# Kernel optimization log

Hardware: AMD Instinct MI355X
Metric: run time of the kernel (lower is better)

## Reference

```python
import jax, jax.numpy as jnp
import numpy as np

N = 30000      # nodes
E = 480000     # edges
NF = 92        # node features
EF = 50        # edge features
D1 = 64        # dim1
D2 = 64        # dim2
L = 3          # conv_count
FC = 2         # fc_count
G = 256        # graphs in batch
EPS = 1e-5


def setup_inputs() -> dict:
    key = jax.random.key(0)
    ks = jax.random.split(key, 20)
    s = 0.05
    zd = 2 * D1 + EF  # CGConv concat dim
    inp = {
        "x": jax.random.normal(ks[0], (N, NF), jnp.float32),
        "edge_attr": jax.random.uniform(ks[1], (E, EF), jnp.float32),
        "lin0_w": jax.random.normal(ks[2], (NF, D1), jnp.float32) * s,
        "lin0_b": jnp.zeros((D1,), jnp.float32),
        "conv_wf": jax.random.normal(ks[3], (L, zd, D1), jnp.float32) * s,
        "conv_bf": jnp.zeros((L, D1), jnp.float32),
        "conv_ws": jax.random.normal(ks[4], (L, zd, D1), jnp.float32) * s,
        "conv_bs": jnp.zeros((L, D1), jnp.float32),
        "bn_gamma": jnp.ones((L, D1), jnp.float32),
        "bn_beta": jnp.zeros((L, D1), jnp.float32),
        "lin1_w": jax.random.normal(ks[5], (D1, D2), jnp.float32) * s,
        "lin1_b": jnp.zeros((D2,), jnp.float32),
        "fc_w": jax.random.normal(ks[6], (FC, D2, D2), jnp.float32) * s,
        "fc_b": jnp.zeros((FC, D2), jnp.float32),
        "lin2_w": jax.random.normal(ks[7], (D2, 1), jnp.float32) * s,
        "lin2_b": jnp.zeros((1,), jnp.float32),
        "edge_index": jax.random.randint(ks[8], (2, E), 0, N),
        "batch": jnp.sort(jax.random.randint(ks[9], (N,), 0, G)),
        "n_graphs": G,
    }
    return inp


def reference(x, edge_attr, lin0_w, lin0_b, conv_wf, conv_bf, conv_ws, conv_bs,
              bn_gamma, bn_beta, lin1_w, lin1_b, fc_w, fc_b, lin2_w, lin2_b,
              edge_index, batch, n_graphs):
    n = x.shape[0]
    src = edge_index[0]  # x_j (source)
    dst = edge_index[1]  # x_i (target, aggregation index)
    h = jax.nn.relu(x @ lin0_w + lin0_b)  # [N, D1]

    # per-target edge counts for mean aggregation (constant across layers)
    cnt = jax.ops.segment_sum(jnp.ones((src.shape[0],), h.dtype), dst, num_segments=n)
    cnt = jnp.maximum(cnt, 1.0)[:, None]

    for l in range(L):
        # z = [x_i || x_j || e_ij]  -> gated message sigmoid(Wf z) * softplus(Ws z)
        z = jnp.concatenate([h[dst], h[src], edge_attr], axis=-1)  # [E, 2*D1+EF]
        m = jax.nn.sigmoid(z @ conv_wf[l] + conv_bf[l]) * jax.nn.softplus(z @ conv_ws[l] + conv_bs[l])
        aggr = jax.ops.segment_sum(m, dst, num_segments=n) / cnt  # mean aggr [N, D1]
        # BatchNorm (training-mode batch stats, biased variance as in torch)
        mu = jnp.mean(aggr, axis=0)
        var = jnp.var(aggr, axis=0)
        aggr = (aggr - mu) * jax.lax.rsqrt(var + EPS) * bn_gamma[l] + bn_beta[l]
        h = jax.nn.relu(h + aggr)  # residual then outer ReLU

    # global mean pool over graphs
    gcnt = jnp.maximum(jax.ops.segment_sum(jnp.ones((n,), h.dtype), batch, num_segments=n_graphs), 1.0)[:, None]
    out = jax.ops.segment_sum(h, batch, num_segments=n_graphs) / gcnt  # [G, D1]

    out = jax.nn.relu(out @ lin1_w + lin1_b)
    for f in range(FC):
        out = jax.nn.relu(out @ fc_w[f] + fc_b[f])
    out = out @ lin2_w + lin2_b
    return out.reshape(-1)  # [G]
```

## Files before the change

kernel.cpp:

```cpp
#include <hip/hip_runtime.h>
#include <hip/hip_bf16.h>

#define N_NODES 30000
#define N_EDGES 480000
#define NFEAT 92
#define EFEAT 50
#define D1 64
#define ZD 178
#define NL 3
#define NG 256
#define BN_EPS 1e-5f
#define NTILES (N_EDGES / 16)
#define EDGE_BLOCKS 7500
#define EDGE_GRID 7504

#define LIN0_BLOCKS 512
#define CNT_BLOCKS 1875
#define WPREP_BLOCKS 96
#define SCAN_BLOCKS ((N_NODES + 255) / 256)
#define BUILD_BLOCKS 1875
#define NP_BLOCKS 1024

typedef __attribute__((ext_vector_type(8))) short bf16x8;
typedef __attribute__((ext_vector_type(8))) unsigned short u16x8;
typedef __attribute__((ext_vector_type(4))) unsigned short u16x4;
typedef __attribute__((ext_vector_type(4))) float f32x4;

static __device__ __forceinline__ unsigned short f2bf(float v) {
  __hip_bfloat16 b = __float2bfloat16(v);
  return *(unsigned short*)&b;
}
static __device__ __forceinline__ float bfu(unsigned short u) {
  union { unsigned int i; float f; } c;
  c.i = ((unsigned int)u) << 16;
  return c.f;
}

static __device__ __forceinline__ void nodeproj_body(
    int blk0, int nblk, const float* __restrict__ hin, float* __restrict__ hout,
    const float* __restrict__ wfp, const float* __restrict__ wsm,
    unsigned short* __restrict__ projd_pk, unsigned short* __restrict__ projs_pk,
    const float* __restrict__ aggr, float* __restrict__ aggr_z,
    const float* __restrict__ invc, const float* __restrict__ musum,
    const float* __restrict__ sqsum, const float* __restrict__ gamma,
    const float* __restrict__ beta, int do_bn, float (*hl)[64]) {
  const int lane = threadIdx.x & 63;
  const int w = threadIdx.x >> 6;
  const float* W = (w < 2) ? wfp : wsm;
  const int roff = (w & 1) * 64;
  float wreg[D1];
#pragma unroll
  for (int k = 0; k < D1; ++k) wreg[k] = W[(size_t)(roff + k) * D1 + lane];
  unsigned short* pk = (w & 1) ? projs_pk : projd_pk;
  const int slot = (w < 2) ? 0 : 4;
  const int poff = (lane >> 2) * 8 + (lane & 3) + slot;
  float r = 0.0f, sh = 0.0f;
  if (do_bn) {
    const float mu = musum[lane] * (1.0f / N_NODES);
    const float var = sqsum[lane] * (1.0f / N_NODES) - mu * mu;
    r = gamma[lane] * rsqrtf(var + BN_EPS);
    sh = beta[lane] - mu * r;
  }
  for (int i = blk0; i < N_NODES; i += nblk) {
    float hv = hin[(size_t)i * D1 + lane];
    if (do_bn) {
      const float av = aggr[(size_t)i * D1 + lane] * invc[i];
      hv = fmaxf(hv + fmaf(av, r, sh), 0.0f);
      if (w == 0) hout[(size_t)i * D1 + lane] = hv;
    }
    if (w == 1) aggr_z[(size_t)i * D1 + lane] = 0.0f;
    hl[w][lane] = hv;
    __builtin_amdgcn_wave_barrier();
    const float4* hr = (const float4*)&hl[w][0];
    float acc = 0.0f;
#pragma unroll
    for (int k4 = 0; k4 < D1 / 4; ++k4) {
      const float4 v = hr[k4];
      acc = fmaf(v.x, wreg[4 * k4 + 0], acc);
      acc = fmaf(v.y, wreg[4 * k4 + 1], acc);
      acc = fmaf(v.z, wreg[4 * k4 + 2], acc);
      acc = fmaf(v.w, wreg[4 * k4 + 3], acc);
    }
    pk[(size_t)i * 128 + poff] = f2bf(acc);
    __builtin_amdgcn_wave_barrier();
  }
}

extern "C" __global__ void __launch_bounds__(256)
k_init(const float* __restrict__ x, const float* __restrict__ w,
       const float* __restrict__ b, float* __restrict__ h,
       const int* __restrict__ ei, int* __restrict__ cnt,
       const float* __restrict__ conv_wf, const float* __restrict__ conv_ws,
       unsigned short* __restrict__ Bp) {
  const int blk = blockIdx.x;
  if (blk < LIN0_BLOCKS) {
    const int lane = threadIdx.x & 63;
    const int wave = (blk * 256 + threadIdx.x) >> 6;
    const int nw = (LIN0_BLOCKS * 256) >> 6;
    float wreg[NFEAT];
#pragma unroll
    for (int k = 0; k < NFEAT; ++k) wreg[k] = w[k * D1 + lane];
    const float bj = b[lane];
    for (int i = wave; i < N_NODES; i += nw) {
      const float2* xr = (const float2*)(x + (size_t)i * NFEAT);
      float acc = bj;
#pragma unroll
      for (int k = 0; k < NFEAT / 2; ++k) {
        const float2 v = xr[k];
        acc = fmaf(v.x, wreg[2 * k], acc);
        acc = fmaf(v.y, wreg[2 * k + 1], acc);
      }
      h[(size_t)i * D1 + lane] = fmaxf(acc, 0.0f);
    }
  } else if (blk < LIN0_BLOCKS + CNT_BLOCKS) {
    const int e = (blk - LIN0_BLOCKS) * 256 + threadIdx.x;
    if (e < N_EDGES) atomicAdd(&cnt[ei[N_EDGES + e]], 1);
  } else {
    const int idx = (blk - LIN0_BLOCKS - CNT_BLOCKS) * 256 + threadIdx.x;
    const int j = idx & 7;
    const int lane = (idx >> 3) & 63;
    const int frag = (idx >> 9) & 15;
    const int l = idx >> 13;
    const int n = frag & 3;
    const int t = (frag >> 2) & 1;
    const int m = frag >> 3;
    const int k = t * 32 + (lane >> 4) * 8 + j;
    const int feat = (lane & 15) * 4 + n;
    float v = 0.0f;
    if (k < EFEAT) {
      const float* W = (m == 0) ? conv_wf : conv_ws;
      v = W[(size_t)l * ZD * D1 + (size_t)(128 + k) * D1 + feat];
    }
    Bp[idx] = f2bf(v);
  }
}

extern "C" __global__ void __launch_bounds__(256)
k_scan1(const int* __restrict__ cnt, int* __restrict__ lpre, int* __restrict__ ptot) {
  const int t = threadIdx.x;
  const int idx = blockIdx.x * 256 + t;
  const int v = (idx < N_NODES) ? cnt[idx] : 0;
  __shared__ int bs[256];
  bs[t] = v;
  __syncthreads();
  for (int off = 1; off < 256; off <<= 1) {
    int u = (t >= off) ? bs[t - off] : 0;
    __syncthreads();
    bs[t] += u;
    __syncthreads();
  }
  if (idx < N_NODES) lpre[idx] = bs[t] - v;
  if (t == 255) ptot[blockIdx.x] = bs[255];
}

extern "C" __global__ void __launch_bounds__(256)
k_scan23(const int* __restrict__ cnt, const int* __restrict__ lpre,
         const int* __restrict__ ptot, const int* __restrict__ batch,
         int* __restrict__ wptr, float* __restrict__ invc,
         int* __restrict__ grp) {
  __shared__ int bs[128];
  const int t = threadIdx.x;
  if (t < 128) bs[t] = (t < SCAN_BLOCKS) ? ptot[t] : 0;
  __syncthreads();
  for (int off = 1; off < 128; off <<= 1) {
    int u = 0;
    if (t < 128 && t >= off) u = bs[t - off];
    __syncthreads();
    if (t < 128 && t >= off) bs[t] += u;
    __syncthreads();
  }
  const int idx = blockIdx.x * 256 + t;
  if (idx >= N_NODES) return;
  const int bid = idx >> 8;
  const int boff = (bid == 0) ? 0 : bs[bid - 1];
  wptr[idx] = boff + lpre[idx];
  invc[idx] = 1.0f / fmaxf((float)cnt[idx], 1.0f);
  const int bt = batch[idx];
  if (idx == 0)
    for (int g = 0; g <= bt; ++g) grp[g] = 0;
  else {
    const int pb = batch[idx - 1];
    for (int g = pb + 1; g <= bt; ++g) grp[g] = idx;
  }
  if (idx == N_NODES - 1)
    for (int g = bt + 1; g <= NG; ++g) grp[g] = N_NODES;
}

extern "C" __global__ void __launch_bounds__(256)
k_build(const int* __restrict__ ei, int* __restrict__ wptr,
        int2* __restrict__ ds2, const float* __restrict__ ea,
        unsigned short* __restrict__ eapb,
        const float* __restrict__ h0, const float* __restrict__ wfl,
        const float* __restrict__ wsl, unsigned short* __restrict__ projd_pk,
        unsigned short* __restrict__ projs_pk, float* __restrict__ aggrA) {
  __shared__ __align__(16) int lpos[256];
  if (blockIdx.x >= BUILD_BLOCKS) {
    nodeproj_body(blockIdx.x - BUILD_BLOCKS, NP_BLOCKS, h0, nullptr, wfl, wsl,
                  projd_pk, projs_pk, nullptr, aggrA, nullptr, nullptr, nullptr,
                  nullptr, nullptr, 0, (float(*)[64])lpos);
    return;
  }
  const int e0 = blockIdx.x * 256;
  {
    const int e = e0 + threadIdx.x;
    const int d = ei[N_EDGES + e];
    const int pos = atomicAdd(&wptr[d], 1);
    ds2[pos] = make_int2(d, ei[e]);
    lpos[threadIdx.x] = pos;
  }
  __syncthreads();
  const int l16 = threadIdx.x & 15;
  const int sub = threadIdx.x >> 4;
#pragma unroll
  for (int r = 0; r < 16; ++r) {
    const int eb = r * 16 + sub;
    const size_t ge = e0 + eb;
    const int pos = lpos[eb];
    unsigned short o0 = 0, o1 = 0, o2 = 0, o3 = 0;
    if (l16 < 12) {
      const float4 v = *(const float4*)(ea + ge * EFEAT + l16 * 4);
      o0 = f2bf(v.x); o1 = f2bf(v.y); o2 = f2bf(v.z); o3 = f2bf(v.w);
    } else if (l16 == 12) {
      const float2 v = *(const float2*)(ea + ge * EFEAT + 48);
      o0 = f2bf(v.x); o1 = f2bf(v.y);
    }
    u16x4 st;
    st[0] = o0; st[1] = o1; st[2] = o2; st[3] = o3;
    *(u16x4*)(eapb + ((size_t)pos << 6) + l16 * 4) = st;
  }
}

extern "C" __global__ void __launch_bounds__(256)
k_nodeproj(const float* __restrict__ hin, float* __restrict__ hout,
           const float* __restrict__ wfp, const float* __restrict__ wsm,
           unsigned short* __restrict__ projd_pk, unsigned short* __restrict__ projs_pk,
           const float* __restrict__ aggr, float* __restrict__ aggr_z,
           const float* __restrict__ invc,
           const float* __restrict__ musum, const float* __restrict__ sqsum,
           const float* __restrict__ gamma, const float* __restrict__ beta) {
  __shared__ float hl[4][64];
  nodeproj_body(blockIdx.x, gridDim.x, hin, hout, wfp, wsm, projd_pk, projs_pk,
                aggr, aggr_z, invc, musum, sqsum, gamma, beta, 1, hl);
}

extern "C" __global__ void __launch_bounds__(256)
k_edgemm(const unsigned short* __restrict__ projd_pk,
         const unsigned short* __restrict__ projs_pk,
         const unsigned short* __restrict__ eapb,
         const int2* __restrict__ ds2,
         const unsigned short* __restrict__ Bp,
         const float* __restrict__ bfp, const float* __restrict__ bsp,
         float* __restrict__ aggr, float* __restrict__ musum,
         float* __restrict__ sqsum) {
  const int lane = threadIdx.x & 63;
  const int wv = threadIdx.x >> 6;
  const int col = lane & 15;
  const int quad = lane >> 4;
  __shared__ float mlds[4][16][68];

  const int vbid = (blockIdx.x & 7) * 938 + (blockIdx.x >> 3);
  if (blockIdx.x == 0 && wv == 0) {
    musum[lane] = 0.0f;
    sqsum[lane] = 0.0f;
  }
  if (vbid >= EDGE_BLOCKS) return;

  const int t = vbid * 4 + wv;
  const int base = t * 16;

  const int4 p01 = *(const int4*)(ds2 + base + quad * 4);
  const int4 p23 = *(const int4*)(ds2 + base + quad * 4 + 2);
  const int dr[4] = {p01.x, p01.z, p23.x, p23.z};
  const int sr[4] = {p01.y, p01.w, p23.y, p23.w};
  const bf16x8 Af0 = *(const bf16x8*)(eapb + ((size_t)(base + col) << 6) + quad * 8);
  const bf16x8 Af1 = *(const bf16x8*)(eapb + ((size_t)(base + col) << 6) + 32 + quad * 8);

  bf16x8 Bf[2][2][4];
#pragma unroll
  for (int m = 0; m < 2; ++m)
#pragma unroll
    for (int tt = 0; tt < 2; ++tt)
#pragma unroll
      for (int n = 0; n < 4; ++n)
        Bf[m][tt][n] = *(const bf16x8*)(Bp + ((((m * 2 + tt) * 4 + n) * 64 + lane) * 8));

  const f32x4 bf4 = *(const f32x4*)(bfp + col * 4);
  const f32x4 bs4 = *(const f32x4*)(bsp + col * 4);

  f32x4 aF[4], aS[4];
#pragma unroll
  for (int r = 0; r < 4; ++r) {
    const int d = dr[r];
    const int s = sr[r];
    const u16x8 pd = *(const u16x8*)(projd_pk + (size_t)d * 128 + col * 8);
    const u16x8 ss = *(const u16x8*)(projs_pk + (size_t)s * 128 + col * 8);
#pragma unroll
    for (int n = 0; n < 4; ++n) {
      aF[n][r] = bfu(pd[n]) + bfu(ss[n]) + bf4[n];
      aS[n][r] = bfu(pd[n + 4]) + bfu(ss[n + 4]) + bs4[n];
    }
  }

#pragma unroll
  for (int n = 0; n < 4; ++n) {
    aF[n] = __builtin_amdgcn_mfma_f32_16x16x32_bf16(Af0, Bf[0][0][n], aF[n], 0, 0, 0);
    aF[n] = __builtin_amdgcn_mfma_f32_16x16x32_bf16(Af1, Bf[0][1][n], aF[n], 0, 0, 0);
    aS[n] = __builtin_amdgcn_mfma_f32_16x16x32_bf16(Af0, Bf[1][0][n], aS[n], 0, 0, 0);
    aS[n] = __builtin_amdgcn_mfma_f32_16x16x32_bf16(Af1, Bf[1][1][n], aS[n], 0, 0, 0);
  }

#pragma unroll
  for (int r = 0; r < 4; ++r) {
    f32x4 mv;
#pragma unroll
    for (int n = 0; n < 4; ++n) {
      const float af = aF[n][r];
      const float as = aS[n][r];
      const float sg = __builtin_amdgcn_rcpf(1.0f + __expf(-af));
      const float sp = fmaxf(as, 0.0f) + __logf(1.0f + __expf(-fabsf(as)));
      mv[n] = sg * sp;
    }
    *(f32x4*)&mlds[wv][quad * 4 + r][col * 4] = mv;
  }
  __builtin_amdgcn_wave_barrier();

  float sum = 0.0f;
  int dcur = ds2[base].x;
#pragma unroll
  for (int p = 0; p < 16; ++p) {
    sum += mlds[wv][p][lane];
    const int dnxt = (p < 15) ? ds2[base + p + 1].x : -1;
    if (dnxt != dcur) {
      atomicAdd(&aggr[(size_t)dcur * D1 + lane], sum);
      sum = 0.0f;
      dcur = dnxt;
    }
  }
}

extern "C" __global__ void __launch_bounds__(256)
k_stats(const float* __restrict__ aggr, const float* __restrict__ invc,
        float* __restrict__ musum, float* __restrict__ sqsum) {
  const int j = threadIdx.x & 63;
  const int rid = (blockIdx.x * blockDim.x + threadIdx.x) >> 6;
  const int rstr = (gridDim.x * blockDim.x) >> 6;
  float s = 0.0f, sq = 0.0f;
  for (int i = rid; i < N_NODES; i += rstr) {
    const float v = aggr[(size_t)i * D1 + j] * invc[i];
    s += v;
    sq = fmaf(v, v, sq);
  }
  __shared__ float ls[256], lq[256];
  ls[threadIdx.x] = s;
  lq[threadIdx.x] = sq;
  __syncthreads();
  if (threadIdx.x < 64) {
    s = ls[j] + ls[64 + j] + ls[128 + j] + ls[192 + j];
    sq = lq[j] + lq[64 + j] + lq[128 + j] + lq[192 + j];
    atomicAdd(&musum[j], s);
    atomicAdd(&sqsum[j], sq);
  }
}

extern "C" __global__ void __launch_bounds__(256)
k_poolmlp(const float* __restrict__ h, const float* __restrict__ aggr,
          const float* __restrict__ invc,
          const float* __restrict__ musum, const float* __restrict__ sqsum,
          const float* __restrict__ gamma, const float* __restrict__ beta,
          const int* __restrict__ grp,
          const float* __restrict__ lin1_w, const float* __restrict__ lin1_b,
          const float* __restrict__ fc_w, const float* __restrict__ fc_b,
          const float* __restrict__ lin2_w, const float* __restrict__ lin2_b,
          float* __restrict__ out) {
  const int g = blockIdx.x;
  const int lane = threadIdx.x & 63;
  const int wv = threadIdx.x >> 6;
  const float mu = musum[lane] * (1.0f / N_NODES);
  const float var = sqsum[lane] * (1.0f / N_NODES) - mu * mu;
  const float r = gamma[lane] * rsqrtf(var + BN_EPS);
  const float sh = beta[lane] - mu * r;
  const int s = grp[g], e = grp[g + 1];
  float acc = 0.0f;
  for (int i = s + wv; i < e; i += 4) {
    const float hv = h[(size_t)i * D1 + lane];
    const float av = aggr[(size_t)i * D1 + lane] * invc[i];
    acc += fmaxf(hv + fmaf(av, r, sh), 0.0f);
  }
  __shared__ float red[4][64];
  __shared__ float vin[64];
  red[wv][lane] = acc;
  __syncthreads();
  const int j = threadIdx.x;
  float v = 0.0f;
  if (j < 64) {
    const float inv = 1.0f / fmaxf((float)(e - s), 1.0f);
    v = (red[0][j] + red[1][j] + red[2][j] + red[3][j]) * inv;
  }
  for (int layer = 0; layer < 3; ++layer) {
    if (j < 64) vin[j] = v;
    __syncthreads();
    if (j < 64) {
      const float* W;
      const float* B;
      if (layer == 0) {
        W = lin1_w;
        B = lin1_b;
      } else {
        W = fc_w + (size_t)(layer - 1) * D1 * D1;
        B = fc_b + (size_t)(layer - 1) * D1;
      }
      float a2 = B[j];
#pragma unroll 16
      for (int k = 0; k < D1; ++k) a2 = fmaf(vin[k], W[k * D1 + j], a2);
      v = fmaxf(a2, 0.0f);
    }
    __syncthreads();
  }
  if (j < 64) {
    float p = v * lin2_w[j];
#pragma unroll
    for (int off = 32; off > 0; off >>= 1) p += __shfl_down(p, off);
    if (j == 0) out[g] = p + lin2_b[0];
  }
}

extern "C" void kernel_launch(void* const* d_in, const int* in_sizes, int n_in,
                              void* d_out, int out_size, void* d_ws, size_t ws_size,
                              hipStream_t stream) {
  const float* x        = (const float*)d_in[0];
  const float* ea       = (const float*)d_in[1];
  const float* lin0_w   = (const float*)d_in[2];
  const float* lin0_b   = (const float*)d_in[3];
  const float* conv_wf  = (const float*)d_in[4];
  const float* conv_bf  = (const float*)d_in[5];
  const float* conv_ws  = (const float*)d_in[6];
  const float* conv_bs  = (const float*)d_in[7];
  const float* bn_gamma = (const float*)d_in[8];
  const float* bn_beta  = (const float*)d_in[9];
  const float* lin1_w   = (const float*)d_in[10];
  const float* lin1_b   = (const float*)d_in[11];
  const float* fc_w     = (const float*)d_in[12];
  const float* fc_b     = (const float*)d_in[13];
  const float* lin2_w   = (const float*)d_in[14];
  const float* lin2_b   = (const float*)d_in[15];
  const int*   ei       = (const int*)d_in[16];
  const int*   batch    = (const int*)d_in[17];

  uintptr_t p = (uintptr_t)d_ws;
  auto alloc = [&](size_t bytes) {
    p = (p + 255) & ~(size_t)255;
    void* r = (void*)p;
    p += bytes;
    return r;
  };
  float* h0     = (float*)alloc((size_t)N_NODES * 64 * 4);
  float* h1     = (float*)alloc((size_t)N_NODES * 64 * 4);
  unsigned short* projd_pk = (unsigned short*)alloc((size_t)N_NODES * 128 * 2);
  unsigned short* projs_pk = (unsigned short*)alloc((size_t)N_NODES * 128 * 2);
  float* aggrA  = (float*)alloc((size_t)N_NODES * 64 * 4);
  float* aggrB  = (float*)alloc((size_t)N_NODES * 64 * 4);
  float* musum  = (float*)alloc(128 * 4);
  float* sqsum  = musum + 64;
  float* invc   = (float*)alloc((size_t)N_NODES * 4);
  int*   cnt    = (int*)alloc((size_t)N_NODES * 4);
  int*   lpre   = (int*)alloc((size_t)N_NODES * 4);
  int*   ptot   = (int*)alloc((size_t)SCAN_BLOCKS * 4);
  int*   wptr   = (int*)alloc((size_t)N_NODES * 4);
  int2*  ds2    = (int2*)alloc((size_t)N_EDGES * 8);
  int*   grp    = (int*)alloc((size_t)(NG + 1) * 4);
  unsigned short* eapb = (unsigned short*)alloc((size_t)N_EDGES * 64 * 2);
  unsigned short* Bp   = (unsigned short*)alloc((size_t)NL * 16 * 64 * 8 * 2);

  hipMemsetAsync(cnt, 0, N_NODES * sizeof(int), stream);
  k_init<<<LIN0_BLOCKS + CNT_BLOCKS + WPREP_BLOCKS, 256, 0, stream>>>(
      x, lin0_w, lin0_b, h0, ei, cnt, conv_wf, conv_ws, Bp);
  k_scan1<<<SCAN_BLOCKS, 256, 0, stream>>>(cnt, lpre, ptot);
  k_scan23<<<SCAN_BLOCKS, 256, 0, stream>>>(cnt, lpre, ptot, batch, wptr, invc, grp);
  k_build<<<BUILD_BLOCKS + NP_BLOCKS, 256, 0, stream>>>(
      ei, wptr, ds2, ea, eapb, h0, conv_wf, conv_ws, projd_pk, projs_pk, aggrA);

  float* aggr_of[NL] = {aggrA, aggrB, aggrA};
  const float* hin_of[NL]  = {h0, h0, h1};
  float* hout_of[NL]       = {h0, h1, h0};

  for (int l = 0; l < NL; ++l) {
    const float* wfl = conv_wf + (size_t)l * ZD * D1;
    const float* wsl = conv_ws + (size_t)l * ZD * D1;
    if (l > 0)
      k_nodeproj<<<1024, 256, 0, stream>>>(
          hin_of[l], hout_of[l], wfl, wsl, projd_pk, projs_pk,
          aggr_of[l - 1], aggr_of[l], invc, musum, sqsum,
          bn_gamma + (size_t)(l - 1) * D1, bn_beta + (size_t)(l - 1) * D1);
    k_edgemm<<<EDGE_GRID, 256, 0, stream>>>(
        projd_pk, projs_pk, eapb, ds2,
        Bp + (size_t)l * 16 * 64 * 8,
        conv_bf + (size_t)l * D1, conv_bs + (size_t)l * D1,
        aggr_of[l], musum, sqsum);
    k_stats<<<256, 256, 0, stream>>>(aggr_of[l], invc, musum, sqsum);
  }

  k_poolmlp<<<NG, 256, 0, stream>>>(h0, aggr_of[2], invc, musum, sqsum,
                                    bn_gamma + (size_t)2 * D1, bn_beta + (size_t)2 * D1,
                                    grp, lin1_w, lin1_b, fc_w, fc_b,
                                    lin2_w, lin2_b, (float*)d_out);
}
```

Before: 621.7 us.

## Store edge attributes in original order and gather them via sorted index

The build kernel now writes packed bf16 edge attributes in original edge order, so the stores are coalesced instead of scattered, and it records each edge's original id in a widened int4 sorted-edge array. The edge kernel then gathers its edge-attribute rows through that id. This cheapens the one-time build and drops the shared-memory sync there. In exchange, each of the three layers' edge kernels reads a twice-as-large index array and does random 128-byte attribute gathers instead of contiguous reads.

```diff
diff --git a/kernel.cpp b/kernel.cpp
--- a/kernel.cpp
+++ b/kernel.cpp
@@ -188,34 +188,29 @@
 
 extern "C" __global__ void __launch_bounds__(256)
 k_build(const int* __restrict__ ei, int* __restrict__ wptr,
-        int2* __restrict__ ds2, const float* __restrict__ ea,
+        int4* __restrict__ ds4, const float* __restrict__ ea,
         unsigned short* __restrict__ eapb,
         const float* __restrict__ h0, const float* __restrict__ wfl,
         const float* __restrict__ wsl, unsigned short* __restrict__ projd_pk,
         unsigned short* __restrict__ projs_pk, float* __restrict__ aggrA) {
-  __shared__ __align__(16) int lpos[256];
+  __shared__ float hl4[4][64];
   if (blockIdx.x >= BUILD_BLOCKS) {
     nodeproj_body(blockIdx.x - BUILD_BLOCKS, NP_BLOCKS, h0, nullptr, wfl, wsl,
                   projd_pk, projs_pk, nullptr, aggrA, nullptr, nullptr, nullptr,
-                  nullptr, nullptr, 0, (float(*)[64])lpos);
+                  nullptr, nullptr, 0, hl4);
     return;
   }
   const int e0 = blockIdx.x * 256;
-  {
-    const int e = e0 + threadIdx.x;
-    const int d = ei[N_EDGES + e];
-    const int pos = atomicAdd(&wptr[d], 1);
-    ds2[pos] = make_int2(d, ei[e]);
-    lpos[threadIdx.x] = pos;
-  }
-  __syncthreads();
+  const int e = e0 + threadIdx.x;
+  const int d = ei[N_EDGES + e];
+  const int s = ei[e];
+  const int pos = atomicAdd(&wptr[d], 1);
+
   const int l16 = threadIdx.x & 15;
   const int sub = threadIdx.x >> 4;
 #pragma unroll
   for (int r = 0; r < 16; ++r) {
-    const int eb = r * 16 + sub;
-    const size_t ge = e0 + eb;
-    const int pos = lpos[eb];
+    const size_t ge = e0 + r * 16 + sub;
     unsigned short o0 = 0, o1 = 0, o2 = 0, o3 = 0;
     if (l16 < 12) {
       const float4 v = *(const float4*)(ea + ge * EFEAT + l16 * 4);
@@ -226,8 +221,10 @@
     }
     u16x4 st;
     st[0] = o0; st[1] = o1; st[2] = o2; st[3] = o3;
-    *(u16x4*)(eapb + ((size_t)pos << 6) + l16 * 4) = st;
-  }
+    *(u16x4*)(eapb + (ge << 6) + l16 * 4) = st;
+  }
+
+  ds4[pos] = make_int4(d, s, e, 0);
 }
 
 extern "C" __global__ void __launch_bounds__(256)
@@ -247,7 +244,7 @@
 k_edgemm(const unsigned short* __restrict__ projd_pk,
          const unsigned short* __restrict__ projs_pk,
          const unsigned short* __restrict__ eapb,
-         const int2* __restrict__ ds2,
+         const int4* __restrict__ ds4,
          const unsigned short* __restrict__ Bp,
          const float* __restrict__ bfp, const float* __restrict__ bsp,
          float* __restrict__ aggr, float* __restrict__ musum,
@@ -268,12 +265,16 @@
   const int t = vbid * 4 + wv;
   const int base = t * 16;
 
-  const int4 p01 = *(const int4*)(ds2 + base + quad * 4);
-  const int4 p23 = *(const int4*)(ds2 + base + quad * 4 + 2);
-  const int dr[4] = {p01.x, p01.z, p23.x, p23.z};
-  const int sr[4] = {p01.y, p01.w, p23.y, p23.w};
-  const bf16x8 Af0 = *(const bf16x8*)(eapb + ((size_t)(base + col) << 6) + quad * 8);
-  const bf16x8 Af1 = *(const bf16x8*)(eapb + ((size_t)(base + col) << 6) + 32 + quad * 8);
+  int dr[4], sr[4];
+#pragma unroll
+  for (int r = 0; r < 4; ++r) {
+    const int4 q = ds4[base + quad * 4 + r];
+    dr[r] = q.x;
+    sr[r] = q.y;
+  }
+  const int oe = ds4[base + col].z;
+  const bf16x8 Af0 = *(const bf16x8*)(eapb + ((size_t)oe << 6) + quad * 8);
+  const bf16x8 Af1 = *(const bf16x8*)(eapb + ((size_t)oe << 6) + 32 + quad * 8);
 
   bf16x8 Bf[2][2][4];
 #pragma unroll
@@ -325,11 +326,11 @@
   __builtin_amdgcn_wave_barrier();
 
   float sum = 0.0f;
-  int dcur = ds2[base].x;
+  int dcur = ds4[base].x;
 #pragma unroll
   for (int p = 0; p < 16; ++p) {
     sum += mlds[wv][p][lane];
-    const int dnxt = (p < 15) ? ds2[base + p + 1].x : -1;
+    const int dnxt = (p < 15) ? ds4[base + p + 1].x : -1;
     if (dnxt != dcur) {
       atomicAdd(&aggr[(size_t)dcur * D1 + lane], sum);
       sum = 0.0f;
@@ -466,7 +467,7 @@
   int*   lpre   = (int*)alloc((size_t)N_NODES * 4);
   int*   ptot   = (int*)alloc((size_t)SCAN_BLOCKS * 4);
   int*   wptr   = (int*)alloc((size_t)N_NODES * 4);
-  int2*  ds2    = (int2*)alloc((size_t)N_EDGES * 8);
+  int4*  ds4    = (int4*)alloc((size_t)N_EDGES * 16);
   int*   grp    = (int*)alloc((size_t)(NG + 1) * 4);
   unsigned short* eapb = (unsigned short*)alloc((size_t)N_EDGES * 64 * 2);
   unsigned short* Bp   = (unsigned short*)alloc((size_t)NL * 16 * 64 * 8 * 2);
@@ -477,7 +478,7 @@
   k_scan1<<<SCAN_BLOCKS, 256, 0, stream>>>(cnt, lpre, ptot);
   k_scan23<<<SCAN_BLOCKS, 256, 0, stream>>>(cnt, lpre, ptot, batch, wptr, invc, grp);
   k_build<<<BUILD_BLOCKS + NP_BLOCKS, 256, 0, stream>>>(
-      ei, wptr, ds2, ea, eapb, h0, conv_wf, conv_ws, projd_pk, projs_pk, aggrA);
+      ei, wptr, ds4, ea, eapb, h0, conv_wf, conv_ws, projd_pk, projs_pk, aggrA);
 
   float* aggr_of[NL] = {aggrA, aggrB, aggrA};
   const float* hin_of[NL]  = {h0, h0, h1};
@@ -492,7 +493,7 @@
           aggr_of[l - 1], aggr_of[l], invc, musum, sqsum,
           bn_gamma + (size_t)(l - 1) * D1, bn_beta + (size_t)(l - 1) * D1);
     k_edgemm<<<EDGE_GRID, 256, 0, stream>>>(
-        projd_pk, projs_pk, eapb, ds2,
+        projd_pk, projs_pk, eapb, ds4,
         Bp + (size_t)l * 16 * 64 * 8,
         conv_bf + (size_t)l * D1, conv_bs + (size_t)l * D1,
         aggr_of[l], musum, sqsum);
```

After: 626.9 us. No clear change (+0.8%).
